# Kernel tuning notes

Measured on AMD Instinct MI355X. Metric: run time of the kernel, lower is better.

Reference implementation:

```python
import jax, jax.numpy as jnp
from jax import lax
import numpy as np

V, E, H, B, L = 50000, 100, 512, 1024, 128


def _gru_params(key, E, H, dtype=jnp.float32):
    k = 1.0 / np.sqrt(H)
    ks = jax.random.split(key, 4)
    Wih = jax.random.uniform(ks[0], (3 * H, E), dtype, -k, k)
    Whh = jax.random.uniform(ks[1], (3 * H, H), dtype, -k, k)
    bih = jax.random.uniform(ks[2], (3 * H,), dtype, -k, k)
    bhh = jax.random.uniform(ks[3], (3 * H,), dtype, -k, k)
    return Wih, Whh, bih, bhh


def setup_inputs() -> dict:
    key = jax.random.key(0)
    kc, kr, kec, ker, kgc, kgr = jax.random.split(key, 6)
    contexts = jax.random.randint(kc, (B, L), 0, V)
    replies = jax.random.randint(kr, (B, L), 0, V)
    ctx_emb = jax.random.uniform(kec, (V, E), jnp.float32, -0.25, 0.25)
    rep_emb = jax.random.uniform(ker, (V, E), jnp.float32, -0.25, 0.25)
    ctx_Wih, ctx_Whh, ctx_bih, ctx_bhh = _gru_params(kgc, E, H)
    rep_Wih, rep_Whh, rep_bih, rep_bhh = _gru_params(kgr, E, H)
    return dict(contexts=contexts, replies=replies,
                ctx_emb=ctx_emb, ctx_Wih=ctx_Wih, ctx_Whh=ctx_Whh, ctx_bih=ctx_bih, ctx_bhh=ctx_bhh,
                rep_emb=rep_emb, rep_Wih=rep_Wih, rep_Whh=rep_Whh, rep_bih=rep_bih, rep_bhh=rep_bhh)


def _gru_backward_last(x, Wih, Whh, bih, bhh):
    """Final hidden of the backward direction of a bidirectional GRU.
    x: [B, L, E] -> h: [B, H]. enc_h_t[-1] in torch == reverse-direction final state,
    i.e. a GRU run over the time-reversed sequence."""
    Bsz = x.shape[0]
    Hh = Whh.shape[1]
    xs = jnp.swapaxes(x, 0, 1)[::-1]  # [L, B, E], reversed time

    def step(h, xt):
        gi = xt @ Wih.T + bih          # [B, 3H]
        gh = h @ Whh.T + bhh           # [B, 3H]
        i_r, i_z, i_n = jnp.split(gi, 3, axis=-1)
        h_r, h_z, h_n = jnp.split(gh, 3, axis=-1)
        r = jax.nn.sigmoid(i_r + h_r)
        z = jax.nn.sigmoid(i_z + h_z)
        n = jnp.tanh(i_n + r * h_n)
        h_new = (1.0 - z) * n + z * h
        return h_new, None

    h0 = jnp.zeros((Bsz, Hh), x.dtype)
    h_last, _ = lax.scan(step, h0, xs)
    return h_last


def reference(contexts, replies,
              ctx_emb, ctx_Wih, ctx_Whh, ctx_bih, ctx_bhh,
              rep_emb, rep_Wih, rep_Whh, rep_bih, rep_bhh):
    # embedding lookup (dropout is identity at eval)
    ex_c = ctx_emb[contexts]  # [B, L, E]
    ex_r = rep_emb[replies]   # [B, L, E]
    hc = _gru_backward_last(ex_c, ctx_Wih, ctx_Whh, ctx_bih, ctx_bhh)  # [B, H]
    hr = _gru_backward_last(ex_r, rep_Wih, rep_Whh, rep_bih, rep_bhh)  # [B, H]
    # fused equivalent of the nested-loop per-pair dot products + row softmax
    scores = hc @ hr.T  # [B, B]
    return jax.nn.softmax(scores, axis=-1)
```

## Files before the change

kernel.cpp:

```cpp
#include <hip/hip_runtime.h>
#include <math.h>

#define B_SZ   1024
#define H_SZ   512
#define E_SZ   100
#define L_SZ   128
#define KX     128
#define VOCAB  50000

typedef _Float16 f16x8  __attribute__((ext_vector_type(8)));
typedef float    f32x4  __attribute__((ext_vector_type(4)));
typedef float    f32x16 __attribute__((ext_vector_type(16)));

#define MFMA16(a, b, c) __builtin_amdgcn_mfma_f32_16x16x32_f16((a), (b), (c), 0, 0, 0)
#define MFMA32(a, b, c) __builtin_amdgcn_mfma_f32_32x32x16_f16((a), (b), (c), 0, 0, 0)

__device__ __forceinline__ float fast_sigmoid(float x) {
    return __builtin_amdgcn_rcpf(1.0f + __expf(-x));
}
__device__ __forceinline__ float fast_tanh(float x) {
    return 1.0f - 2.0f * __builtin_amdgcn_rcpf(1.0f + __expf(2.0f * x));
}

__global__ __launch_bounds__(256) void prep_emb_kernel(
    _Float16* __restrict__ ef_c, const float* __restrict__ e_c,
    _Float16* __restrict__ ef_r, const float* __restrict__ e_r)
{
    const int PER = VOCAB * KX;
    int idx = blockIdx.x * 256 + threadIdx.x;
    if (idx >= 2 * PER) return;
    const int gru = idx >= PER;
    const int local = gru ? idx - PER : idx;
    const int v = local >> 7;
    const int e = local & 127;
    const float* src = gru ? e_r : e_c;
    _Float16* dst = gru ? ef_r : ef_c;
    dst[local] = (_Float16)(e < E_SZ ? src[v * E_SZ + e] : 0.0f);
}

struct GruArgs {
    const float* Whh[2];
    const float* Wih[2];
    const float* bih[2];
    const float* bhh[2];
    const _Float16* emb[2];
    const int* idx[2];
    _Float16* hA;
    _Float16* hB;
    unsigned int* bars;
    unsigned int* claim;
};

__global__ __launch_bounds__(256, 1) void gru_persistent(GruArgs args)
{
    __shared__ int role_s;
    if (threadIdx.x == 0) {
        unsigned xcd;
        asm volatile("s_getreg_b32 %0, hwreg(HW_REG_XCC_ID)" : "=s"(xcd));
        xcd &= 7u;
        unsigned slot = atomicAdd(&args.claim[xcd], 1u);
        role_s = (int)(xcd * 32u + slot);
    }
    __syncthreads();
    const int role = role_s;
    const int grp  = role >> 4;
    const int ut   = role & 15;
    const int gru  = grp >> 3;
    const int mt   = grp & 7;

    const float* __restrict__ Whh = args.Whh[gru];
    const float* __restrict__ Wih = args.Wih[gru];
    const float* __restrict__ bih = args.bih[gru];
    const float* __restrict__ bhh = args.bhh[gru];
    const _Float16* __restrict__ embf = args.emb[gru];
    const int* __restrict__ idx = args.idx[gru];

    const int u0 = ut * 32;
    const int mB = mt * 128;

    __shared__ _Float16 Wl[7680 * 8];

    for (int f = threadIdx.x; f < 7680; f += 256) {
        const int ln  = f & 63;
        const int q   = f >> 6;
        const int kc  = q / 3;
        const int g   = q - kc * 3;
        const int col = ln & 31;
        const int kh  = ln >> 5;
        const int row = g * H_SZ + u0 + col;
        _Float16 tmp[8];
        if (kc < 32) {
            const float* src = Whh + (size_t)row * H_SZ + kc * 16 + kh * 8;
#pragma unroll
            for (int j = 0; j < 8; ++j) tmp[j] = (_Float16)src[j];
        } else {
            const int e = (kc - 32) * 16 + kh * 8;
#pragma unroll
            for (int j = 0; j < 8; ++j)
                tmp[j] = (_Float16)((e + j < E_SZ) ? Wih[(size_t)row * E_SZ + e + j]
                                                   : 0.0f);
        }
        *(f16x8*)&Wl[(size_t)f * 8] = *(const f16x8*)tmp;
    }
    __syncthreads();

    const int lane = threadIdx.x & 63;
    const int wave = threadIdx.x >> 6;
    const int lr   = lane & 31;
    const int kh   = lane >> 5;
    const int mw   = mB + wave * 32;

    const _Float16* Wbase = Wl + (size_t)lane * 8;
#define WFRAG(kc, g) \
    (*(const f16x8*)(Wbase + (size_t)(((kc) * 3 + (g)) * 64) * 8))

    const int ucol = u0 + lr;
    const float bir  = bih[ucol]            + bhh[ucol];
    const float biz  = bih[H_SZ + ucol]     + bhh[H_SZ + ucol];
    const float binn = bih[2 * H_SZ + ucol];
    const float bhn  = bhh[2 * H_SZ + ucol];

    _Float16* hbuf0 = args.hA + (size_t)gru * B_SZ * H_SZ;
    _Float16* hbuf1 = args.hB + (size_t)gru * B_SZ * H_SZ;
    unsigned int* bar = args.bars + grp * 32;

    float hreg[16] = {};

    f16x8 er[8];
    int ivn;
    {
        const int iv_c = idx[(mw + lr) * L_SZ + (L_SZ - 1)];
        const _Float16* e0 = embf + (size_t)iv_c * KX + kh * 8;
#pragma unroll
        for (int xc = 0; xc < 8; ++xc)
            er[xc] = *(const f16x8*)(e0 + xc * 16);
        ivn = idx[(mw + lr) * L_SZ + (L_SZ - 2)];
    }

#pragma unroll 1
    for (int step = 0; step < L_SZ; ++step) {
        const _Float16* __restrict__ hin = (step & 1) ? hbuf1 : hbuf0;
        _Float16* __restrict__ hout      = (step & 1) ? hbuf0 : hbuf1;

        f32x16 accr  = {0.f,0.f,0.f,0.f,0.f,0.f,0.f,0.f,0.f,0.f,0.f,0.f,0.f,0.f,0.f,0.f};
        f32x16 accz  = {0.f,0.f,0.f,0.f,0.f,0.f,0.f,0.f,0.f,0.f,0.f,0.f,0.f,0.f,0.f,0.f};
        f32x16 acchn = {0.f,0.f,0.f,0.f,0.f,0.f,0.f,0.f,0.f,0.f,0.f,0.f,0.f,0.f,0.f,0.f};
        f32x16 accin = {0.f,0.f,0.f,0.f,0.f,0.f,0.f,0.f,0.f,0.f,0.f,0.f,0.f,0.f,0.f,0.f};

#pragma unroll
        for (int xc = 0; xc < 8; ++xc) {
            accr  = MFMA32(er[xc], WFRAG(32 + xc, 0), accr);
            accz  = MFMA32(er[xc], WFRAG(32 + xc, 1), accz);
            accin = MFMA32(er[xc], WFRAG(32 + xc, 2), accin);
        }

        if (step > 0) {
            if (threadIdx.x == 0) {
                const unsigned tgt = 16u * (unsigned)step;
                while (__hip_atomic_load(bar, __ATOMIC_RELAXED,
                                         __HIP_MEMORY_SCOPE_AGENT) < tgt)
                    __builtin_amdgcn_s_sleep(1);
            }
            __syncthreads();
        }

        const _Float16* hrow0 = hin + (mw + lr) * H_SZ + kh * 8;
        f16x8 a0h[32];
        asm volatile(
            "global_load_dwordx4 %0,  %32, off sc0\n\t"
            "global_load_dwordx4 %1,  %32, off offset:32 sc0\n\t"
            "global_load_dwordx4 %2,  %32, off offset:64 sc0\n\t"
            "global_load_dwordx4 %3,  %32, off offset:96 sc0\n\t"
            "global_load_dwordx4 %4,  %32, off offset:128 sc0\n\t"
            "global_load_dwordx4 %5,  %32, off offset:160 sc0\n\t"
            "global_load_dwordx4 %6,  %32, off offset:192 sc0\n\t"
            "global_load_dwordx4 %7,  %32, off offset:224 sc0\n\t"
            "global_load_dwordx4 %8,  %32, off offset:256 sc0\n\t"
            "global_load_dwordx4 %9,  %32, off offset:288 sc0\n\t"
            "global_load_dwordx4 %10, %32, off offset:320 sc0\n\t"
            "global_load_dwordx4 %11, %32, off offset:352 sc0\n\t"
            "global_load_dwordx4 %12, %32, off offset:384 sc0\n\t"
            "global_load_dwordx4 %13, %32, off offset:416 sc0\n\t"
            "global_load_dwordx4 %14, %32, off offset:448 sc0\n\t"
            "global_load_dwordx4 %15, %32, off offset:480 sc0\n\t"
            "global_load_dwordx4 %16, %32, off offset:512 sc0\n\t"
            "global_load_dwordx4 %17, %32, off offset:544 sc0\n\t"
            "global_load_dwordx4 %18, %32, off offset:576 sc0\n\t"
            "global_load_dwordx4 %19, %32, off offset:608 sc0\n\t"
            "global_load_dwordx4 %20, %32, off offset:640 sc0\n\t"
            "global_load_dwordx4 %21, %32, off offset:672 sc0\n\t"
            "global_load_dwordx4 %22, %32, off offset:704 sc0\n\t"
            "global_load_dwordx4 %23, %32, off offset:736 sc0\n\t"
            "global_load_dwordx4 %24, %32, off offset:768 sc0\n\t"
            "global_load_dwordx4 %25, %32, off offset:800 sc0\n\t"
            "global_load_dwordx4 %26, %32, off offset:832 sc0\n\t"
            "global_load_dwordx4 %27, %32, off offset:864 sc0\n\t"
            "global_load_dwordx4 %28, %32, off offset:896 sc0\n\t"
            "global_load_dwordx4 %29, %32, off offset:928 sc0\n\t"
            "global_load_dwordx4 %30, %32, off offset:960 sc0\n\t"
            "global_load_dwordx4 %31, %32, off offset:992 sc0\n\t"
            "s_waitcnt vmcnt(0)"
            : "=&v"(a0h[0]),  "=&v"(a0h[1]),  "=&v"(a0h[2]),  "=&v"(a0h[3]),
              "=&v"(a0h[4]),  "=&v"(a0h[5]),  "=&v"(a0h[6]),  "=&v"(a0h[7]),
              "=&v"(a0h[8]),  "=&v"(a0h[9]),  "=&v"(a0h[10]), "=&v"(a0h[11]),
              "=&v"(a0h[12]), "=&v"(a0h[13]), "=&v"(a0h[14]), "=&v"(a0h[15]),
              "=&v"(a0h[16]), "=&v"(a0h[17]), "=&v"(a0h[18]), "=&v"(a0h[19]),
              "=&v"(a0h[20]), "=&v"(a0h[21]), "=&v"(a0h[22]), "=&v"(a0h[23]),
              "=&v"(a0h[24]), "=&v"(a0h[25]), "=&v"(a0h[26]), "=&v"(a0h[27]),
              "=&v"(a0h[28]), "=&v"(a0h[29]), "=&v"(a0h[30]), "=&v"(a0h[31])
            : "v"(hrow0)
            : "memory");

        {
            const _Float16* erow = embf + (size_t)ivn * KX + kh * 8;
#pragma unroll
            for (int xc = 0; xc < 8; ++xc)
                er[xc] = *(const f16x8*)(erow + xc * 16);
            int lc = L_SZ - 3 - step;
            if (lc < 0) lc = 0;
            ivn = idx[(mw + lr) * L_SZ + lc];
        }

#pragma unroll
        for (int kc = 0; kc < 32; ++kc) {
            accr  = MFMA32(a0h[kc], WFRAG(kc, 0), accr);
            accz  = MFMA32(a0h[kc], WFRAG(kc, 1), accz);
            acchn = MFMA32(a0h[kc], WFRAG(kc, 2), acchn);
        }

#pragma unroll
        for (int r = 0; r < 16; ++r) {
            const int m = mw + (r & 3) + 8 * (r >> 2) + 4 * kh;
            const float rg = fast_sigmoid(accr[r] + bir);
            const float zg = fast_sigmoid(accz[r] + biz);
            const float ng = fast_tanh(accin[r] + binn +
                                       rg * (acchn[r] + bhn));
            float nh = (1.0f - zg) * ng + zg * hreg[r];
            nh = (float)(_Float16)nh;
            hreg[r] = nh;
            hout[m * H_SZ + ucol] = (_Float16)nh;
        }

        if (step + 1 < L_SZ) {
            __syncthreads();
            if (threadIdx.x == 0) {
                __hip_atomic_fetch_add(bar, 1u, __ATOMIC_RELAXED,
                                       __HIP_MEMORY_SCOPE_AGENT);
            }
        }
    }
    asm volatile("s_waitcnt vmcnt(0)" ::: "memory");
#undef WFRAG
}

__global__ __launch_bounds__(256, 1) void scores_kernel(
    const _Float16* __restrict__ hc, const _Float16* __restrict__ hr,
    float* __restrict__ out)
{
    const int lane = threadIdx.x & 63;
    const int wave = threadIdx.x >> 6;
    const int lr   = lane & 15;
    const int kseg = lane >> 4;
    const int m0 = blockIdx.y * 64 + (wave >> 1) * 32;
    const int n0 = blockIdx.x * 64 + (wave & 1) * 32;

    f32x4 acc[2][2];
#pragma unroll
    for (int i = 0; i < 2; i++)
#pragma unroll
        for (int j = 0; j < 2; j++)
            acc[i][j] = (f32x4){0.f, 0.f, 0.f, 0.f};

#pragma unroll 2
    for (int kc = 0; kc < 16; kc++) {
        const int k0 = kc * 32 + kseg * 8;
        f16x8 a[2], b[2];
#pragma unroll
        for (int mt = 0; mt < 2; mt++)
            a[mt] = *(const f16x8*)(hc + (m0 + mt * 16 + lr) * H_SZ + k0);
#pragma unroll
        for (int nt = 0; nt < 2; nt++)
            b[nt] = *(const f16x8*)(hr + (n0 + nt * 16 + lr) * H_SZ + k0);
#pragma unroll
        for (int mt = 0; mt < 2; mt++)
#pragma unroll
            for (int nt = 0; nt < 2; nt++)
                acc[mt][nt] = MFMA16(a[mt], b[nt], acc[mt][nt]);
    }

#pragma unroll
    for (int mt = 0; mt < 2; mt++)
#pragma unroll
        for (int nt = 0; nt < 2; nt++)
#pragma unroll
            for (int r = 0; r < 4; r++) {
                const int m = m0 + mt * 16 + kseg * 4 + r;
                const int n = n0 + nt * 16 + lr;
                out[m * B_SZ + n] = acc[mt][nt][r];
            }
}

__global__ __launch_bounds__(256) void softmax_kernel(float* __restrict__ out)
{
    const int row = blockIdx.x;
    float* p = out + (size_t)row * B_SZ;
    const int t = threadIdx.x;
    const int wave = t >> 6;
    const int lane = t & 63;

    float4 v = ((const float4*)p)[t];
    float m = fmaxf(fmaxf(v.x, v.y), fmaxf(v.z, v.w));
#pragma unroll
    for (int off = 32; off >= 1; off >>= 1)
        m = fmaxf(m, __shfl_xor(m, off, 64));

    __shared__ float redm[4];
    if (lane == 0) redm[wave] = m;
    __syncthreads();
    m = fmaxf(fmaxf(redm[0], redm[1]), fmaxf(redm[2], redm[3]));

    const float e0 = __expf(v.x - m);
    const float e1 = __expf(v.y - m);
    const float e2 = __expf(v.z - m);
    const float e3 = __expf(v.w - m);
    float s = e0 + e1 + e2 + e3;
#pragma unroll
    for (int off = 32; off >= 1; off >>= 1)
        s += __shfl_xor(s, off, 64);

    __shared__ float reds[4];
    if (lane == 0) reds[wave] = s;
    __syncthreads();
    s = reds[0] + reds[1] + reds[2] + reds[3];

    const float inv = 1.0f / s;
    float4 o;
    o.x = e0 * inv; o.y = e1 * inv; o.z = e2 * inv; o.w = e3 * inv;
    ((float4*)p)[t] = o;
}

extern "C" void kernel_launch(void* const* d_in, const int* in_sizes, int n_in,
                              void* d_out, int out_size, void* d_ws, size_t ws_size,
                              hipStream_t stream)
{
    (void)in_sizes; (void)n_in; (void)out_size; (void)ws_size;

    const int*   contexts = (const int*)d_in[0];
    const int*   replies  = (const int*)d_in[1];
    const float* ctx_emb  = (const float*)d_in[2];
    const float* ctx_Wih  = (const float*)d_in[3];
    const float* ctx_Whh  = (const float*)d_in[4];
    const float* ctx_bih  = (const float*)d_in[5];
    const float* ctx_bhh  = (const float*)d_in[6];
    const float* rep_emb  = (const float*)d_in[7];
    const float* rep_Wih  = (const float*)d_in[8];
    const float* rep_Whh  = (const float*)d_in[9];
    const float* rep_bih  = (const float*)d_in[10];
    const float* rep_bhh  = (const float*)d_in[11];
    float* out = (float*)d_out;

    const size_t EMB_ELEMS = (size_t)VOCAB * KX;
    const size_t H_ELEMS   = (size_t)B_SZ * H_SZ;

    _Float16* base   = (_Float16*)d_ws;
    _Float16* embf_c = base;
    _Float16* embf_r = embf_c + EMB_ELEMS;
    _Float16* hB     = embf_r + EMB_ELEMS;
    _Float16* hA     = hB + 2 * H_ELEMS;
    unsigned int* bars  = (unsigned int*)(hA + 2 * H_ELEMS);
    unsigned int* claim = bars + 16 * 32;

    hipMemsetAsync(hA, 0,
                   2 * H_ELEMS * sizeof(_Float16) +
                   (16 * 32 + 8) * sizeof(unsigned int), stream);

    {
        const int total_emb = 2 * (int)EMB_ELEMS;
        prep_emb_kernel<<<(total_emb + 255) / 256, 256, 0, stream>>>(
            embf_c, ctx_emb, embf_r, rep_emb);
    }

    GruArgs a;
    a.Whh[0] = ctx_Whh; a.Whh[1] = rep_Whh;
    a.Wih[0] = ctx_Wih; a.Wih[1] = rep_Wih;
    a.bih[0] = ctx_bih; a.bih[1] = rep_bih;
    a.bhh[0] = ctx_bhh; a.bhh[1] = rep_bhh;
    a.emb[0] = embf_c;  a.emb[1] = embf_r;
    a.idx[0] = contexts; a.idx[1] = replies;
    a.hA = hA; a.hB = hB; a.bars = bars; a.claim = claim;
    gru_persistent<<<dim3(256), dim3(256), 0, stream>>>(a);

    scores_kernel<<<dim3(B_SZ / 64, B_SZ / 64), 256, 0, stream>>>(hA, hA + H_ELEMS, out);
    softmax_kernel<<<B_SZ, 256, 0, stream>>>(out);
}
```

Before: 1.162 ms.

## Split GRU recurrent K-reduction across wave pairs with LDS partial-sum exchange

Doubles the persistent GRU block to 512 threads so that each row tile is handled by two waves, each covering half of the hidden and embedding K dimension. Partial accumulators are combined through a shared-memory buffer, using extra block barriers, before one wave of each pair applies the gate nonlinearities and writes h. The aim is to shorten the per-step serial MFMA chain and halve per-wave register pressure and h-load volume on the latency-bound recurrence. In exchange it adds three __syncthreads and LDS traffic per step, plus extra LDS capacity.

```diff
diff --git a/kernel.cpp b/kernel.cpp
--- a/kernel.cpp
+++ b/kernel.cpp
@@ -51,7 +51,7 @@
     unsigned int* claim;
 };
 
-__global__ __launch_bounds__(256, 1) void gru_persistent(GruArgs args)
+__global__ __launch_bounds__(512, 2) void gru_persistent(GruArgs args)
 {
     __shared__ int role_s;
     if (threadIdx.x == 0) {
@@ -79,8 +79,9 @@
     const int mB = mt * 128;
 
     __shared__ _Float16 Wl[7680 * 8];
-
-    for (int f = threadIdx.x; f < 7680; f += 256) {
+    __shared__ float2 xb[16][4][64];
+
+    for (int f = threadIdx.x; f < 7680; f += 512) {
         const int ln  = f & 63;
         const int q   = f >> 6;
         const int kc  = q / 3;
@@ -106,9 +107,11 @@
 
     const int lane = threadIdx.x & 63;
     const int wave = threadIdx.x >> 6;
+    const int rg   = wave >> 1;
+    const int wk   = wave & 1;
     const int lr   = lane & 31;
-    const int kh   = lane >> 5;
-    const int mw   = mB + wave * 32;
+    const int kh2  = lane >> 5;
+    const int mw   = mB + rg * 32;
 
     const _Float16* Wbase = Wl + (size_t)lane * 8;
 #define WFRAG(kc, g) \
@@ -126,14 +129,14 @@
 
     float hreg[16] = {};
 
-    f16x8 er[8];
+    f16x8 er[4];
     int ivn;
     {
         const int iv_c = idx[(mw + lr) * L_SZ + (L_SZ - 1)];
-        const _Float16* e0 = embf + (size_t)iv_c * KX + kh * 8;
-#pragma unroll
-        for (int xc = 0; xc < 8; ++xc)
-            er[xc] = *(const f16x8*)(e0 + xc * 16);
+        const _Float16* e0 = embf + (size_t)iv_c * KX + wk * 64 + kh2 * 8;
+#pragma unroll
+        for (int i = 0; i < 4; ++i)
+            er[i] = *(const f16x8*)(e0 + i * 16);
         ivn = idx[(mw + lr) * L_SZ + (L_SZ - 2)];
     }
 
@@ -148,10 +151,11 @@
         f32x16 accin = {0.f,0.f,0.f,0.f,0.f,0.f,0.f,0.f,0.f,0.f,0.f,0.f,0.f,0.f,0.f,0.f};
 
 #pragma unroll
-        for (int xc = 0; xc < 8; ++xc) {
-            accr  = MFMA32(er[xc], WFRAG(32 + xc, 0), accr);
-            accz  = MFMA32(er[xc], WFRAG(32 + xc, 1), accz);
-            accin = MFMA32(er[xc], WFRAG(32 + xc, 2), accin);
+        for (int i = 0; i < 4; ++i) {
+            const int kc = 32 + wk * 4 + i;
+            accr  = MFMA32(er[i], WFRAG(kc, 0), accr);
+            accz  = MFMA32(er[i], WFRAG(kc, 1), accz);
+            accin = MFMA32(er[i], WFRAG(kc, 2), accin);
         }
 
         if (step > 0) {
@@ -164,81 +168,96 @@
             __syncthreads();
         }
 
-        const _Float16* hrow0 = hin + (mw + lr) * H_SZ + kh * 8;
-        f16x8 a0h[32];
+        const _Float16* hrow0 = hin + (mw + lr) * H_SZ + wk * 256 + kh2 * 8;
+        f16x8 a0h[16];
         asm volatile(
-            "global_load_dwordx4 %0,  %32, off sc0\n\t"
-            "global_load_dwordx4 %1,  %32, off offset:32 sc0\n\t"
-            "global_load_dwordx4 %2,  %32, off offset:64 sc0\n\t"
-            "global_load_dwordx4 %3,  %32, off offset:96 sc0\n\t"
-            "global_load_dwordx4 %4,  %32, off offset:128 sc0\n\t"
-            "global_load_dwordx4 %5,  %32, off offset:160 sc0\n\t"
-            "global_load_dwordx4 %6,  %32, off offset:192 sc0\n\t"
-            "global_load_dwordx4 %7,  %32, off offset:224 sc0\n\t"
-            "global_load_dwordx4 %8,  %32, off offset:256 sc0\n\t"
-            "global_load_dwordx4 %9,  %32, off offset:288 sc0\n\t"
-            "global_load_dwordx4 %10, %32, off offset:320 sc0\n\t"
-            "global_load_dwordx4 %11, %32, off offset:352 sc0\n\t"
-            "global_load_dwordx4 %12, %32, off offset:384 sc0\n\t"
-            "global_load_dwordx4 %13, %32, off offset:416 sc0\n\t"
-            "global_load_dwordx4 %14, %32, off offset:448 sc0\n\t"
-            "global_load_dwordx4 %15, %32, off offset:480 sc0\n\t"
-            "global_load_dwordx4 %16, %32, off offset:512 sc0\n\t"
-            "global_load_dwordx4 %17, %32, off offset:544 sc0\n\t"
-            "global_load_dwordx4 %18, %32, off offset:576 sc0\n\t"
-            "global_load_dwordx4 %19, %32, off offset:608 sc0\n\t"
-            "global_load_dwordx4 %20, %32, off offset:640 sc0\n\t"
-            "global_load_dwordx4 %21, %32, off offset:672 sc0\n\t"
-            "global_load_dwordx4 %22, %32, off offset:704 sc0\n\t"
-            "global_load_dwordx4 %23, %32, off offset:736 sc0\n\t"
-            "global_load_dwordx4 %24, %32, off offset:768 sc0\n\t"
-            "global_load_dwordx4 %25, %32, off offset:800 sc0\n\t"
-            "global_load_dwordx4 %26, %32, off offset:832 sc0\n\t"
-            "global_load_dwordx4 %27, %32, off offset:864 sc0\n\t"
-            "global_load_dwordx4 %28, %32, off offset:896 sc0\n\t"
-            "global_load_dwordx4 %29, %32, off offset:928 sc0\n\t"
-            "global_load_dwordx4 %30, %32, off offset:960 sc0\n\t"
-            "global_load_dwordx4 %31, %32, off offset:992 sc0\n\t"
+            "global_load_dwordx4 %0,  %16, off sc0\n\t"
+            "global_load_dwordx4 %1,  %16, off offset:32 sc0\n\t"
+            "global_load_dwordx4 %2,  %16, off offset:64 sc0\n\t"
+            "global_load_dwordx4 %3,  %16, off offset:96 sc0\n\t"
+            "global_load_dwordx4 %4,  %16, off offset:128 sc0\n\t"
+            "global_load_dwordx4 %5,  %16, off offset:160 sc0\n\t"
+            "global_load_dwordx4 %6,  %16, off offset:192 sc0\n\t"
+            "global_load_dwordx4 %7,  %16, off offset:224 sc0\n\t"
+            "global_load_dwordx4 %8,  %16, off offset:256 sc0\n\t"
+            "global_load_dwordx4 %9,  %16, off offset:288 sc0\n\t"
+            "global_load_dwordx4 %10, %16, off offset:320 sc0\n\t"
+            "global_load_dwordx4 %11, %16, off offset:352 sc0\n\t"
+            "global_load_dwordx4 %12, %16, off offset:384 sc0\n\t"
+            "global_load_dwordx4 %13, %16, off offset:416 sc0\n\t"
+            "global_load_dwordx4 %14, %16, off offset:448 sc0\n\t"
+            "global_load_dwordx4 %15, %16, off offset:480 sc0\n\t"
             "s_waitcnt vmcnt(0)"
             : "=&v"(a0h[0]),  "=&v"(a0h[1]),  "=&v"(a0h[2]),  "=&v"(a0h[3]),
               "=&v"(a0h[4]),  "=&v"(a0h[5]),  "=&v"(a0h[6]),  "=&v"(a0h[7]),
               "=&v"(a0h[8]),  "=&v"(a0h[9]),  "=&v"(a0h[10]), "=&v"(a0h[11]),
-              "=&v"(a0h[12]), "=&v"(a0h[13]), "=&v"(a0h[14]), "=&v"(a0h[15]),
-              "=&v"(a0h[16]), "=&v"(a0h[17]), "=&v"(a0h[18]), "=&v"(a0h[19]),
-              "=&v"(a0h[20]), "=&v"(a0h[21]), "=&v"(a0h[22]), "=&v"(a0h[23]),
-              "=&v"(a0h[24]), "=&v"(a0h[25]), "=&v"(a0h[26]), "=&v"(a0h[27]),
-              "=&v"(a0h[28]), "=&v"(a0h[29]), "=&v"(a0h[30]), "=&v"(a0h[31])
+              "=&v"(a0h[12]), "=&v"(a0h[13]), "=&v"(a0h[14]), "=&v"(a0h[15])
             : "v"(hrow0)
             : "memory");
 
         {
-            const _Float16* erow = embf + (size_t)ivn * KX + kh * 8;
-#pragma unroll
-            for (int xc = 0; xc < 8; ++xc)
-                er[xc] = *(const f16x8*)(erow + xc * 16);
+            const _Float16* erow = embf + (size_t)ivn * KX + wk * 64 + kh2 * 8;
+#pragma unroll
+            for (int i = 0; i < 4; ++i)
+                er[i] = *(const f16x8*)(erow + i * 16);
             int lc = L_SZ - 3 - step;
             if (lc < 0) lc = 0;
             ivn = idx[(mw + lr) * L_SZ + lc];
         }
 
 #pragma unroll
-        for (int kc = 0; kc < 32; ++kc) {
-            accr  = MFMA32(a0h[kc], WFRAG(kc, 0), accr);
-            accz  = MFMA32(a0h[kc], WFRAG(kc, 1), accz);
-            acchn = MFMA32(a0h[kc], WFRAG(kc, 2), acchn);
-        }
-
-#pragma unroll
-        for (int r = 0; r < 16; ++r) {
-            const int m = mw + (r & 3) + 8 * (r >> 2) + 4 * kh;
-            const float rg = fast_sigmoid(accr[r] + bir);
-            const float zg = fast_sigmoid(accz[r] + biz);
-            const float ng = fast_tanh(accin[r] + binn +
-                                       rg * (acchn[r] + bhn));
-            float nh = (1.0f - zg) * ng + zg * hreg[r];
-            nh = (float)(_Float16)nh;
-            hreg[r] = nh;
-            hout[m * H_SZ + ucol] = (_Float16)nh;
+        for (int j = 0; j < 16; ++j) {
+            const int kc = wk * 16 + j;
+            accr  = MFMA32(a0h[j], WFRAG(kc, 0), accr);
+            accz  = MFMA32(a0h[j], WFRAG(kc, 1), accz);
+            acchn = MFMA32(a0h[j], WFRAG(kc, 2), acchn);
+        }
+
+        if (wk == 1) {
+#pragma unroll
+            for (int p = 0; p < 8; ++p) {
+                xb[p][rg][lane]     = make_float2(accr[2*p], accr[2*p+1]);
+                xb[8 + p][rg][lane] = make_float2(accz[2*p], accz[2*p+1]);
+            }
+        }
+        __syncthreads();
+        if (wk == 0) {
+#pragma unroll
+            for (int p = 0; p < 8; ++p) {
+                float2 a = xb[p][rg][lane];
+                float2 b = xb[8 + p][rg][lane];
+                accr[2*p] += a.x;  accr[2*p+1] += a.y;
+                accz[2*p] += b.x;  accz[2*p+1] += b.y;
+            }
+        }
+        __syncthreads();
+        if (wk == 1) {
+#pragma unroll
+            for (int p = 0; p < 8; ++p) {
+                xb[p][rg][lane]     = make_float2(acchn[2*p], acchn[2*p+1]);
+                xb[8 + p][rg][lane] = make_float2(accin[2*p], accin[2*p+1]);
+            }
+        }
+        __syncthreads();
+
+        if (wk == 0) {
+#pragma unroll
+            for (int r = 0; r < 16; ++r) {
+                const int p = r >> 1;
+                const float hnp = (r & 1) ? xb[p][rg][lane].y
+                                          : xb[p][rg][lane].x;
+                const float inp = (r & 1) ? xb[8 + p][rg][lane].y
+                                          : xb[8 + p][rg][lane].x;
+                const int m = mw + (r & 3) + 8 * (r >> 2) + 4 * kh2;
+                const float rg_ = fast_sigmoid(accr[r] + bir);
+                const float zg  = fast_sigmoid(accz[r] + biz);
+                const float ng  = fast_tanh(accin[r] + inp + binn +
+                                            rg_ * (acchn[r] + hnp + bhn));
+                float nh = (1.0f - zg) * ng + zg * hreg[r];
+                nh = (float)(_Float16)nh;
+                hreg[r] = nh;
+                hout[m * H_SZ + ucol] = (_Float16)nh;
+            }
         }
 
         if (step + 1 < L_SZ) {
@@ -388,7 +407,7 @@
     a.emb[0] = embf_c;  a.emb[1] = embf_r;
     a.idx[0] = contexts; a.idx[1] = replies;
     a.hA = hA; a.hB = hB; a.bars = bars; a.claim = claim;
-    gru_persistent<<<dim3(256), dim3(256), 0, stream>>>(a);
+    gru_persistent<<<dim3(256), dim3(512), 0, stream>>>(a);
 
     scores_kernel<<<dim3(B_SZ / 64, B_SZ / 64), 256, 0, stream>>>(hA, hA + H_ELEMS, out);
     softmax_kernel<<<B_SZ, 256, 0, stream>>>(out);
```

Result: slower. 1.287 ms (+10.7%).
